# Optimization experiments

Hardware: AMD Instinct MI355X
Metric: run time of the kernel (lower is better)

## Reference

```python
import jax, jax.numpy as jnp
from jax import lax
import numpy as np

PN_FEAT = 64


def _conv(x, w, b):
    # x: [B,H,W,Cin], w: [kh,kw,Cin,Cout] (SAME padding, stride 1)
    return lax.conv_general_dilated(x, w, (1, 1), 'SAME',
                                    dimension_numbers=('NHWC', 'HWIO', 'NHWC')) + b


def setup_inputs() -> dict:
    key = jax.random.key(0)
    ks = jax.random.split(key, 12)
    B, P, N, C = 4, 5000, 100, 8
    nx = ny = 240
    pillars = jax.random.normal(ks[0], (B, P, N, C), dtype=jnp.float32)
    pillar_idxs = jax.random.randint(ks[1], (B, P, 2), 0, nx).astype(jnp.int32)
    def lin(k, fi, fo):
        return jax.random.normal(k, (fi, fo), dtype=jnp.float32) / np.sqrt(fi).astype(np.float32)
    def cnv(k, kh, kw, ci, co):
        return jax.random.normal(k, (kh, kw, ci, co), dtype=jnp.float32) / np.sqrt(kh * kw * ci).astype(np.float32)
    return {
        'pillars': pillars,
        'pillar_idxs': pillar_idxs,
        'nx': nx,
        'ny': ny,
        # pointnet MLP: 8 -> 64 (tanh) -> 64
        'pn_w0': lin(ks[2], 8, 64), 'pn_b0': jnp.zeros((64,), jnp.float32),
        'pn_w1': lin(ks[3], 64, PN_FEAT), 'pn_b1': jnp.zeros((PN_FEAT,), jnp.float32),
        # resnet costmap CNN: 64 -> 128 (tanh) -> 128 (tanh) -> 1, relu output
        'cw0': cnv(ks[4], 3, 3, PN_FEAT, 128), 'cb0': jnp.zeros((128,), jnp.float32),
        'cw1': cnv(ks[5], 3, 3, 128, 128), 'cb1': jnp.zeros((128,), jnp.float32),
        'cw2': cnv(ks[6], 1, 1, 128, 1), 'cb2': jnp.zeros((1,), jnp.float32),
    }


def reference(pillars, pillar_idxs, nx, ny,
              pn_w0, pn_b0, pn_w1, pn_b1,
              cw0, cb0, cw1, cb1, cw2, cb2):
    VALID_THRESH = 1000000.0
    ACT_SCALE = 1.0
    # mask padded points (norm >= 1e6 means invalid)
    valid = (jnp.linalg.norm(pillars, axis=-1, keepdims=True) < VALID_THRESH).astype(pillars.dtype)
    # per-point MLP: [B,P,N,8] -> [B,P,N,F]
    h = jnp.tanh(pillars @ pn_w0 + pn_b0)
    feat = h @ pn_w1 + pn_b1
    # masked max over points in each pillar -> [B,P,F]
    pmax = jnp.max(feat * valid, axis=-2)
    # scatter pillar features into BEV pseudo-image [B,nx,ny,F]
    B = pillars.shape[0]
    bidx = jnp.arange(B)[:, None]                      # [B,1]
    img = jnp.zeros((B, nx, ny, PN_FEAT), pillars.dtype)
    img = img.at[bidx, pillar_idxs[..., 0], pillar_idxs[..., 1]].set(pmax)
    # costmap CNN head (NHWC internally; original is NCHW, same math)
    x = jnp.tanh(_conv(img, cw0, cb0))
    x = jnp.tanh(_conv(x, cw1, cb1))
    x = _conv(x, cw2, cb2)
    return jax.nn.relu(x) * ACT_SCALE            # [B,nx,ny,1]
```

## Files before the change

kernel.cpp:

```cpp
#include <hip/hip_runtime.h>
#include <hip/hip_bf16.h>
#include <math.h>

#define B  4
#define P  5000
#define NPT 100
#define F  64
#define NX 240
#define NY 240
#define C1 128

typedef __attribute__((ext_vector_type(8)))  short short8;
typedef __attribute__((ext_vector_type(16))) float f32x16;

__device__ __forceinline__ float tanh_fast(float x) {
    float e = __expf(2.0f * x);
    float r = __builtin_amdgcn_rcpf(e + 1.0f);
    return __builtin_fmaf(-2.0f, r, 1.0f);
}
__device__ __forceinline__ short bf16_bits(float f) {
    return (short)(__bfloat16_as_ushort(__float2bfloat16(f)));
}

__global__ __launch_bounds__(128) void pn_mfma_kernel(
    const float* __restrict__ pillars,
    const float* __restrict__ w0,
    const float* __restrict__ b0,
    const __hip_bfloat16* __restrict__ w1t,
    const float* __restrict__ b1,
    float* __restrict__ pmax)
{
    constexpr int HS = F + 8;
    constexpr int XS = 32;
    __shared__ short xA[128 * XS];
    __shared__ short hA[128 * HS];
    __shared__ float vmask[128];
    __shared__ float red[2][F];

    int bp = blockIdx.x;
    int n  = threadIdx.x;
    bool live = (n < NPT);

    const float* xp = pillars + ((size_t)bp * NPT + (live ? n : 0)) * 8;
    float4 q0 = *(const float4*)xp;
    float4 q1 = *(const float4*)(xp + 4);
    float x[8] = {q0.x, q0.y, q0.z, q0.w, q1.x, q1.y, q1.z, q1.w};

    float ss = 0.f;
#pragma unroll
    for (int c = 0; c < 8; c++) ss += x[c] * x[c];
    vmask[n] = live ? ((ss < 1e12f) ? 1.0f : 0.0f) : -1.0f;

    short8 xhi, xlo, xz;
#pragma unroll
    for (int c = 0; c < 8; c++) {
        __hip_bfloat16 hb = __float2bfloat16(x[c]);
        float hv = __bfloat162float(hb);
        xhi[c] = (short)__bfloat16_as_ushort(hb);
        xlo[c] = bf16_bits(x[c] - hv);
        xz[c] = 0;
    }
    *(short8*)&xA[n * XS + 0]  = xhi;
    *(short8*)&xA[n * XS + 8]  = xlo;
    *(short8*)&xA[n * XS + 16] = xhi;
    *(short8*)&xA[n * XS + 24] = xz;
    __syncthreads();

    int wave = n >> 6, lane = n & 63;
    int mr = lane & 31;
    int g  = lane >> 5;

    short8 wb[2][2];
#pragma unroll
    for (int nt = 0; nt < 2; nt++) {
        int nn = nt * 32 + mr;
#pragma unroll
        for (int j = 0; j < 8; j++) {
            float wv = w0[j * F + nn];
            __hip_bfloat16 hb = __float2bfloat16(wv);
            wb[0][nt][j] = (short)__bfloat16_as_ushort(hb);
            wb[1][nt][j] = (g == 0) ? bf16_bits(wv - __bfloat162float(hb)) : (short)0;
        }
    }

    f32x16 hc00 = {0,0,0,0,0,0,0,0,0,0,0,0,0,0,0,0};
    f32x16 hc01 = hc00, hc10 = hc00, hc11 = hc00;
#pragma unroll
    for (int kk = 0; kk < 2; kk++) {
        short8 a0 = *(const short8*)&xA[(wave * 64 + mr) * XS + kk * 16 + g * 8];
        short8 a1 = *(const short8*)&xA[(wave * 64 + 32 + mr) * XS + kk * 16 + g * 8];
        hc00 = __builtin_amdgcn_mfma_f32_32x32x16_bf16(a0, wb[kk][0], hc00, 0, 0, 0);
        hc01 = __builtin_amdgcn_mfma_f32_32x32x16_bf16(a0, wb[kk][1], hc01, 0, 0, 0);
        hc10 = __builtin_amdgcn_mfma_f32_32x32x16_bf16(a1, wb[kk][0], hc10, 0, 0, 0);
        hc11 = __builtin_amdgcn_mfma_f32_32x32x16_bf16(a1, wb[kk][1], hc11, 0, 0, 0);
    }

    float b00 = b0[mr];
    float b01 = b0[32 + mr];
#pragma unroll
    for (int mt = 0; mt < 2; mt++) {
#pragma unroll
        for (int r = 0; r < 16; r++) {
            int prow = wave * 64 + mt * 32 + (r & 3) + 8 * (r >> 2) + 4 * g;
            float h0 = (mt == 0) ? hc00[r] : hc10[r];
            float h1 = (mt == 0) ? hc01[r] : hc11[r];
            hA[prow * HS + mr]      = bf16_bits(tanh_fast(h0 + b00));
            hA[prow * HS + 32 + mr] = bf16_bits(tanh_fast(h1 + b01));
        }
    }
    __syncthreads();

    short8 bfrag[2][4];
#pragma unroll
    for (int nt = 0; nt < 2; nt++)
#pragma unroll
        for (int c0 = 0; c0 < 4; c0++)
            bfrag[nt][c0] = *(const short8*)((const short*)w1t +
                                (nt * 32 + mr) * F + c0 * 16 + g * 8);

    f32x16 acc00 = {0,0,0,0,0,0,0,0,0,0,0,0,0,0,0,0};
    f32x16 acc01 = acc00, acc10 = acc00, acc11 = acc00;

    const short* arow = &hA[(wave * 64 + mr) * HS + g * 8];
#pragma unroll
    for (int c0 = 0; c0 < 4; c0++) {
        short8 af0 = *(const short8*)(arow + c0 * 16);
        short8 af1 = *(const short8*)(arow + 32 * HS + c0 * 16);
        acc00 = __builtin_amdgcn_mfma_f32_32x32x16_bf16(af0, bfrag[0][c0], acc00, 0, 0, 0);
        acc01 = __builtin_amdgcn_mfma_f32_32x32x16_bf16(af0, bfrag[1][c0], acc01, 0, 0, 0);
        acc10 = __builtin_amdgcn_mfma_f32_32x32x16_bf16(af1, bfrag[0][c0], acc10, 0, 0, 0);
        acc11 = __builtin_amdgcn_mfma_f32_32x32x16_bf16(af1, bfrag[1][c0], acc11, 0, 0, 0);
    }

    float bv0 = b1[mr];
    float bv1 = b1[32 + mr];
    float mx0 = -INFINITY, mx1 = -INFINITY;
#pragma unroll
    for (int mt = 0; mt < 2; mt++) {
#pragma unroll
        for (int r = 0; r < 16; r++) {
            int row = (r & 3) + 8 * (r >> 2) + 4 * g;
            int p = wave * 64 + mt * 32 + row;
            float vm = vmask[p];
            float a0 = (mt == 0) ? acc00[r] : acc10[r];
            float a1 = (mt == 0) ? acc01[r] : acc11[r];
            float v0 = (vm < 0.f) ? -INFINITY : (a0 + bv0) * vm;
            float v1 = (vm < 0.f) ? -INFINITY : (a1 + bv1) * vm;
            mx0 = fmaxf(mx0, v0);
            mx1 = fmaxf(mx1, v1);
        }
    }
    mx0 = fmaxf(mx0, __shfl_xor(mx0, 32, 64));
    mx1 = fmaxf(mx1, __shfl_xor(mx1, 32, 64));
    if (lane < 32) { red[wave][mr] = mx0; red[wave][32 + mr] = mx1; }
    __syncthreads();
    if (n < F)
        pmax[(size_t)bp * F + n] = fmaxf(red[0][n], red[1][n]);
}

__global__ __launch_bounds__(256) void winner_kernel(
    const int* __restrict__ idxs, int* __restrict__ winner)
{
    int i = blockIdx.x * 256 + threadIdx.x;
    if (i >= B * P) return;
    int ix = idxs[i * 2], iy = idxs[i * 2 + 1];
    int b = i / P, p = i % P;
    atomicMax(&winner[(b * NX + ix) * NY + iy], p);
}

__global__ __launch_bounds__(64) void scatter_kernel(
    const int* __restrict__ idxs, const int* __restrict__ winner,
    const float* __restrict__ pmax, __hip_bfloat16* __restrict__ img)
{
    int bp = blockIdx.x;
    int f = threadIdx.x;
    int ix = idxs[bp * 2], iy = idxs[bp * 2 + 1];
    int b = bp / P, p = bp % P;
    int cell = (b * NX + ix) * NY + iy;
    if (winner[cell] == p)
        img[(size_t)cell * F + f] = __float2bfloat16(pmax[(size_t)bp * F + f]);
}

__global__ __launch_bounds__(256) void cvt_w_kernel(
    const float* __restrict__ w, __hip_bfloat16* __restrict__ wt, int cin)
{
    int idx = blockIdx.x * 256 + threadIdx.x;
    int total = 9 * cin * 128;
    if (idx >= total) return;
    int co = idx % 128;
    int rest = idx / 128;
    int ci = rest % cin;
    int t  = rest / cin;
    int c0 = ci >> 4, c16 = ci & 15;
    wt[(((size_t)(t * (cin >> 4) + c0)) * 128 + co) * 16 + c16] = __float2bfloat16(w[idx]);
}

__global__ __launch_bounds__(256) void cvt_w1_kernel(
    const float* __restrict__ w1, __hip_bfloat16* __restrict__ w1t)
{
    int idx = blockIdx.x * 256 + threadIdx.x;
    if (idx >= F * F) return;
    int k = idx >> 6, nn = idx & 63;
    w1t[nn * F + k] = __float2bfloat16(w1[idx]);
}

template<int CIN, bool FUSE>
__global__ __launch_bounds__(256) void conv_mfma(
    const __hip_bfloat16* __restrict__ in,
    const __hip_bfloat16* __restrict__ wt,
    const float* __restrict__ bias,
    const float* __restrict__ w2,
    const float* __restrict__ b2,
    __hip_bfloat16* __restrict__ out_bf,
    float* __restrict__ out_f)
{
    constexpr int CPAD = CIN + 8;
    constexpr int NC16 = CIN / 16;
    constexpr int NC8  = CIN / 8;
    __shared__ __hip_bfloat16 sP[4 * 66 * CPAD];
    __shared__ float sred[4][64];

    int tid  = threadIdx.x;
    int wave = tid >> 6;
    int lane = tid & 63;
    int mr = lane & 31;
    int g  = lane >> 5;
    int xr  = wave & 1;
    int coh = wave >> 1;
    int y0 = blockIdx.x * 64;
    int x0 = blockIdx.y * 2;
    int b  = blockIdx.z;
    int n0 = coh * 64;

    for (int t = tid; t < 4 * 66 * NC8; t += 256) {
        int c8  = t & (NC8 - 1);
        int row = t / NC8;
        int dy  = row % 66;
        int dx  = row / 66;
        int gx = x0 + dx - 1, gy = y0 + dy - 1;
        float4 v = make_float4(0.f, 0.f, 0.f, 0.f);
        if (gx >= 0 && gx < NX && gy >= 0 && gy < NY)
            v = *(const float4*)&in[(((size_t)b * NX + gx) * NY + gy) * CIN + c8 * 8];
        *(float4*)&sP[row * CPAD + c8 * 8] = v;
    }

    const short* wts = (const short*)wt;
    short8 wbuf[2][NC16][2];
#pragma unroll
    for (int c0 = 0; c0 < NC16; c0++)
#pragma unroll
        for (int nt = 0; nt < 2; nt++)
            wbuf[0][c0][nt] = *(const short8*)(wts +
                ((size_t)c0 * 128 + n0 + nt * 32 + mr) * 16 + g * 8);

    __syncthreads();

    f32x16 acc00 = {0,0,0,0,0,0,0,0,0,0,0,0,0,0,0,0};
    f32x16 acc01 = acc00, acc10 = acc00, acc11 = acc00;
    const short* sPs = (const short*)sP;

#pragma unroll
    for (int tap = 0; tap < 9; tap++) {
        int kh = tap / 3, kw = tap % 3;
        int cur = tap & 1;
        if (tap < 8) {
#pragma unroll
            for (int c0 = 0; c0 < NC16; c0++)
#pragma unroll
                for (int nt = 0; nt < 2; nt++)
                    wbuf[cur ^ 1][c0][nt] = *(const short8*)(wts +
                        ((size_t)((tap + 1) * NC16 + c0) * 128 + n0 + nt * 32 + mr) * 16 + g * 8);
        }
        int prow = ((xr + kh) * 66 + kw + mr) * CPAD + g * 8;
#pragma unroll
        for (int c0 = 0; c0 < NC16; c0++) {
            short8 a0 = *(const short8*)(sPs + prow + c0 * 16);
            short8 a1 = *(const short8*)(sPs + prow + 32 * CPAD + c0 * 16);
            acc00 = __builtin_amdgcn_mfma_f32_32x32x16_bf16(a0, wbuf[cur][c0][0], acc00, 0, 0, 0);
            acc01 = __builtin_amdgcn_mfma_f32_32x32x16_bf16(a0, wbuf[cur][c0][1], acc01, 0, 0, 0);
            acc10 = __builtin_amdgcn_mfma_f32_32x32x16_bf16(a1, wbuf[cur][c0][0], acc10, 0, 0, 0);
            acc11 = __builtin_amdgcn_mfma_f32_32x32x16_bf16(a1, wbuf[cur][c0][1], acc11, 0, 0, 0);
        }
    }

    float bv0 = bias[n0 + mr];
    float bv1 = bias[n0 + 32 + mr];
    int gx = x0 + xr;
    if (!FUSE) {
        size_t base = (((size_t)b * NX + gx) * NY);
#pragma unroll
        for (int mt = 0; mt < 2; mt++) {
#pragma unroll
            for (int r = 0; r < 16; r++) {
                float a0 = (mt == 0) ? acc00[r] : acc10[r];
                float a1 = (mt == 0) ? acc01[r] : acc11[r];
                int row = (r & 3) + 8 * (r >> 2) + 4 * g;
                int y = y0 + mt * 32 + row;
                if (y < NY) {
                    out_bf[(base + y) * C1 + n0 + mr]      = __float2bfloat16(tanh_fast(a0 + bv0));
                    out_bf[(base + y) * C1 + n0 + 32 + mr] = __float2bfloat16(tanh_fast(a1 + bv1));
                }
            }
        }
    } else {
        float w20 = w2[n0 + mr];
        float w21 = w2[n0 + 32 + mr];
#pragma unroll
        for (int mt = 0; mt < 2; mt++) {
#pragma unroll
            for (int r = 0; r < 16; r++) {
                float a0 = (mt == 0) ? acc00[r] : acc10[r];
                float a1 = (mt == 0) ? acc01[r] : acc11[r];
                float v = tanh_fast(a0 + bv0) * w20 + tanh_fast(a1 + bv1) * w21;
                v += __shfl_xor(v, 1, 64);
                v += __shfl_xor(v, 2, 64);
                v += __shfl_xor(v, 4, 64);
                v += __shfl_xor(v, 8, 64);
                v += __shfl_xor(v, 16, 64);
                if (mr == 0) {
                    int row = (r & 3) + 8 * (r >> 2) + 4 * g;
                    sred[wave][mt * 32 + row] = v;
                }
            }
        }
        __syncthreads();
        if (tid < 128) {
            int xr2 = tid >> 6;
            int yy  = tid & 63;
            int y = y0 + yy;
            if (y < NY) {
                float r = sred[xr2][yy] + sred[2 + xr2][yy] + b2[0];
                out_f[((size_t)b * NX + x0 + xr2) * NY + y] = fmaxf(r, 0.f);
            }
        }
    }
}

extern "C" void kernel_launch(void* const* d_in, const int* in_sizes, int n_in,
                              void* d_out, int out_size, void* d_ws, size_t ws_size,
                              hipStream_t stream) {
    const float* pillars = (const float*)d_in[0];
    const int*   idxs    = (const int*)d_in[1];
    const float* pn_w0   = (const float*)d_in[4];
    const float* pn_b0   = (const float*)d_in[5];
    const float* pn_w1   = (const float*)d_in[6];
    const float* pn_b1   = (const float*)d_in[7];
    const float* cw0     = (const float*)d_in[8];
    const float* cb0     = (const float*)d_in[9];
    const float* cw1     = (const float*)d_in[10];
    const float* cb1     = (const float*)d_in[11];
    const float* cw2     = (const float*)d_in[12];
    const float* cb2     = (const float*)d_in[13];
    float* out = (float*)d_out;

    char* ws = (char*)d_ws;
    const size_t IMG_BYTES  = (size_t)B * NX * NY * F * 2;
    const size_t OUT1_BYTES = (size_t)B * NX * NY * C1 * 2;
    const size_t WIN_BYTES  = (size_t)B * NX * NY * 4;
    const size_t PMAX_BYTES = (size_t)B * P * F * 4;
    const size_t WT1_BYTES  = (size_t)9 * C1 * F * 2;
    const size_t WT2_BYTES  = (size_t)9 * C1 * C1 * 2;
    __hip_bfloat16* img  = (__hip_bfloat16*)ws;
    __hip_bfloat16* out1 = (__hip_bfloat16*)(ws + IMG_BYTES);
    int*   winner = (int*)(ws + IMG_BYTES + OUT1_BYTES);
    float* pmax   = (float*)(ws + IMG_BYTES + OUT1_BYTES + WIN_BYTES);
    __hip_bfloat16* wt1 = (__hip_bfloat16*)(ws + IMG_BYTES + OUT1_BYTES + WIN_BYTES + PMAX_BYTES);
    __hip_bfloat16* wt2 = (__hip_bfloat16*)(ws + IMG_BYTES + OUT1_BYTES + WIN_BYTES + PMAX_BYTES + WT1_BYTES);
    __hip_bfloat16* w1t = (__hip_bfloat16*)(ws + IMG_BYTES + OUT1_BYTES + WIN_BYTES + PMAX_BYTES + WT1_BYTES + WT2_BYTES);

    hipMemsetAsync(img, 0, IMG_BYTES, stream);
    hipMemsetAsync(winner, 0xFF, WIN_BYTES, stream);

    cvt_w_kernel<<<(9 * F * C1 + 255) / 256, 256, 0, stream>>>(cw0, wt1, F);
    cvt_w_kernel<<<(9 * C1 * C1 + 255) / 256, 256, 0, stream>>>(cw1, wt2, C1);
    cvt_w1_kernel<<<(F * F + 255) / 256, 256, 0, stream>>>(pn_w1, w1t);

    pn_mfma_kernel<<<B * P, 128, 0, stream>>>(pillars, pn_w0, pn_b0, w1t, pn_b1, pmax);
    winner_kernel<<<(B * P + 255) / 256, 256, 0, stream>>>(idxs, winner);
    scatter_kernel<<<B * P, 64, 0, stream>>>(idxs, winner, pmax, img);

    conv_mfma<F, false><<<dim3(4, NX / 2, B), 256, 0, stream>>>(
        img, wt1, cb0, nullptr, nullptr, out1, nullptr);
    conv_mfma<C1, true><<<dim3(4, NX / 2, B), 256, 0, stream>>>(
        out1, wt2, cb1, cw2, cb2, nullptr, out);
}
```

Baseline: 391.7 us.

## Retile conv kernels to 128-row wave tiles with channel-split LDS passes

Each wave now accumulates a 128x64 output tile (4x2 MFMA accumulators) instead of 64x64, so every weight fragment loaded from global memory feeds twice as many MFMAs. The input halo is staged in LDS in 64-channel passes, which keeps LDS at about 75 KB per block even for the 128-channel conv, and launch_bounds asks for 2 blocks per CU. The grid becomes 120x2 blocks, each covering 112-row-strided y windows of 128 rows, so rows 112-127 are computed twice and the bounds checks are dropped. The trade-off is higher register pressure from 8 accumulators and an extra barrier and reload between channel passes.

```diff
diff --git a/kernel.cpp b/kernel.cpp
--- a/kernel.cpp
+++ b/kernel.cpp
@@ -205,7 +205,7 @@
 }
 
 template<int CIN, bool FUSE>
-__global__ __launch_bounds__(256) void conv_mfma(
+__global__ __launch_bounds__(256, 2) void conv_mfma(
     const __hip_bfloat16* __restrict__ in,
     const __hip_bfloat16* __restrict__ wt,
     const float* __restrict__ bias,
@@ -214,124 +214,131 @@
     __hip_bfloat16* __restrict__ out_bf,
     float* __restrict__ out_f)
 {
-    constexpr int CPAD = CIN + 8;
-    constexpr int NC16 = CIN / 16;
-    constexpr int NC8  = CIN / 8;
-    __shared__ __hip_bfloat16 sP[4 * 66 * CPAD];
-    __shared__ float sred[4][64];
+    constexpr int PASSES = CIN / 64;
+    constexpr int CI   = 64;
+    constexpr int CPAD = CI + 8;
+    constexpr int NC16 = CI / 16;
+    constexpr int NC8  = CI / 8;
+    constexpr int ROWS = 4 * 130;
+    __shared__ short sP[ROWS * CPAD];
+    __shared__ float sred[FUSE ? 2 : 1][2][128];
 
     int tid  = threadIdx.x;
     int wave = tid >> 6;
     int lane = tid & 63;
     int mr = lane & 31;
     int g  = lane >> 5;
-    int xr  = wave & 1;
-    int coh = wave >> 1;
-    int y0 = blockIdx.x * 64;
-    int x0 = blockIdx.y * 2;
+    int coh = wave & 1;
+    int xr  = wave >> 1;
+    int x0 = blockIdx.x * 2;
+    int y0 = blockIdx.y * 112;
     int b  = blockIdx.z;
     int n0 = coh * 64;
 
-    for (int t = tid; t < 4 * 66 * NC8; t += 256) {
-        int c8  = t & (NC8 - 1);
-        int row = t / NC8;
-        int dy  = row % 66;
-        int dx  = row / 66;
-        int gx = x0 + dx - 1, gy = y0 + dy - 1;
-        float4 v = make_float4(0.f, 0.f, 0.f, 0.f);
-        if (gx >= 0 && gx < NX && gy >= 0 && gy < NY)
-            v = *(const float4*)&in[(((size_t)b * NX + gx) * NY + gy) * CIN + c8 * 8];
-        *(float4*)&sP[row * CPAD + c8 * 8] = v;
-    }
-
     const short* wts = (const short*)wt;
+
+    f32x16 acc[4][2];
+#pragma unroll
+    for (int mt = 0; mt < 4; mt++)
+#pragma unroll
+        for (int nt = 0; nt < 2; nt++)
+            acc[mt][nt] = (f32x16){0,0,0,0,0,0,0,0,0,0,0,0,0,0,0,0};
+
     short8 wbuf[2][NC16][2];
 #pragma unroll
     for (int c0 = 0; c0 < NC16; c0++)
 #pragma unroll
         for (int nt = 0; nt < 2; nt++)
             wbuf[0][c0][nt] = *(const short8*)(wts +
-                ((size_t)c0 * 128 + n0 + nt * 32 + mr) * 16 + g * 8);
-
-    __syncthreads();
-
-    f32x16 acc00 = {0,0,0,0,0,0,0,0,0,0,0,0,0,0,0,0};
-    f32x16 acc01 = acc00, acc10 = acc00, acc11 = acc00;
-    const short* sPs = (const short*)sP;
-
-#pragma unroll
-    for (int tap = 0; tap < 9; tap++) {
-        int kh = tap / 3, kw = tap % 3;
-        int cur = tap & 1;
-        if (tap < 8) {
-#pragma unroll
-            for (int c0 = 0; c0 < NC16; c0++)
-#pragma unroll
-                for (int nt = 0; nt < 2; nt++)
-                    wbuf[cur ^ 1][c0][nt] = *(const short8*)(wts +
-                        ((size_t)((tap + 1) * NC16 + c0) * 128 + n0 + nt * 32 + mr) * 16 + g * 8);
-        }
-        int prow = ((xr + kh) * 66 + kw + mr) * CPAD + g * 8;
-#pragma unroll
-        for (int c0 = 0; c0 < NC16; c0++) {
-            short8 a0 = *(const short8*)(sPs + prow + c0 * 16);
-            short8 a1 = *(const short8*)(sPs + prow + 32 * CPAD + c0 * 16);
-            acc00 = __builtin_amdgcn_mfma_f32_32x32x16_bf16(a0, wbuf[cur][c0][0], acc00, 0, 0, 0);
-            acc01 = __builtin_amdgcn_mfma_f32_32x32x16_bf16(a0, wbuf[cur][c0][1], acc01, 0, 0, 0);
-            acc10 = __builtin_amdgcn_mfma_f32_32x32x16_bf16(a1, wbuf[cur][c0][0], acc10, 0, 0, 0);
-            acc11 = __builtin_amdgcn_mfma_f32_32x32x16_bf16(a1, wbuf[cur][c0][1], acc11, 0, 0, 0);
+                ((0 * (CIN / 16) + c0) * 128 + n0 + nt * 32 + mr) * 16 + g * 8);
+
+#pragma unroll
+    for (int p = 0; p < PASSES; p++) {
+        if (p) __syncthreads();
+
+#pragma unroll 4
+        for (int i = 0; i < 17; i++) {
+            int t = tid + i * 256;
+            if (t < ROWS * NC8) {
+                int c8 = t & (NC8 - 1);
+                int r  = t >> 3;
+                int dx = r / 130, dy = r - dx * 130;
+                int gx = x0 - 1 + dx, gy = y0 - 1 + dy;
+                float4 v = make_float4(0.f, 0.f, 0.f, 0.f);
+                if (gx >= 0 && gx < NX && gy >= 0 && gy < NY)
+                    v = *(const float4*)&in[(((size_t)b * NX + gx) * NY + gy) * CIN + p * CI + c8 * 8];
+                *(float4*)&sP[r * CPAD + c8 * 8] = v;
+            }
+        }
+        __syncthreads();
+
+#pragma unroll
+        for (int tap = 0; tap < 9; tap++) {
+            int s = p * 9 + tap;
+            int cur = s & 1;
+            if (s + 1 < 9 * PASSES) {
+                int sn = s + 1, pn_ = sn / 9, tn = sn % 9;
+#pragma unroll
+                for (int c0 = 0; c0 < NC16; c0++)
+#pragma unroll
+                    for (int nt = 0; nt < 2; nt++)
+                        wbuf[cur ^ 1][c0][nt] = *(const short8*)(wts +
+                            ((tn * (CIN / 16) + pn_ * NC16 + c0) * 128 + n0 + nt * 32 + mr) * 16 + g * 8);
+            }
+            int kh = tap / 3, kw = tap % 3;
+            const short* abase = sP + ((xr + kh) * 130 + kw + mr) * CPAD + g * 8;
+#pragma unroll
+            for (int c0 = 0; c0 < NC16; c0++) {
+                short8 a[4];
+#pragma unroll
+                for (int mt = 0; mt < 4; mt++)
+                    a[mt] = *(const short8*)(abase + mt * 32 * CPAD + c0 * 16);
+#pragma unroll
+                for (int mt = 0; mt < 4; mt++) {
+                    acc[mt][0] = __builtin_amdgcn_mfma_f32_32x32x16_bf16(a[mt], wbuf[cur][c0][0], acc[mt][0], 0, 0, 0);
+                    acc[mt][1] = __builtin_amdgcn_mfma_f32_32x32x16_bf16(a[mt], wbuf[cur][c0][1], acc[mt][1], 0, 0, 0);
+                }
+            }
         }
     }
 
     float bv0 = bias[n0 + mr];
     float bv1 = bias[n0 + 32 + mr];
-    int gx = x0 + xr;
     if (!FUSE) {
-        size_t base = (((size_t)b * NX + gx) * NY);
-#pragma unroll
-        for (int mt = 0; mt < 2; mt++) {
+        size_t base = ((size_t)b * NX + (x0 + xr)) * NY;
+#pragma unroll
+        for (int mt = 0; mt < 4; mt++) {
 #pragma unroll
             for (int r = 0; r < 16; r++) {
-                float a0 = (mt == 0) ? acc00[r] : acc10[r];
-                float a1 = (mt == 0) ? acc01[r] : acc11[r];
-                int row = (r & 3) + 8 * (r >> 2) + 4 * g;
-                int y = y0 + mt * 32 + row;
-                if (y < NY) {
-                    out_bf[(base + y) * C1 + n0 + mr]      = __float2bfloat16(tanh_fast(a0 + bv0));
-                    out_bf[(base + y) * C1 + n0 + 32 + mr] = __float2bfloat16(tanh_fast(a1 + bv1));
-                }
+                int y = y0 + mt * 32 + (r & 3) + 8 * (r >> 2) + 4 * g;
+                out_bf[(base + y) * C1 + n0 + mr]      = __float2bfloat16(tanh_fast(acc[mt][0][r] + bv0));
+                out_bf[(base + y) * C1 + n0 + 32 + mr] = __float2bfloat16(tanh_fast(acc[mt][1][r] + bv1));
             }
         }
     } else {
         float w20 = w2[n0 + mr];
         float w21 = w2[n0 + 32 + mr];
 #pragma unroll
-        for (int mt = 0; mt < 2; mt++) {
+        for (int mt = 0; mt < 4; mt++) {
 #pragma unroll
             for (int r = 0; r < 16; r++) {
-                float a0 = (mt == 0) ? acc00[r] : acc10[r];
-                float a1 = (mt == 0) ? acc01[r] : acc11[r];
-                float v = tanh_fast(a0 + bv0) * w20 + tanh_fast(a1 + bv1) * w21;
+                float v = tanh_fast(acc[mt][0][r] + bv0) * w20
+                        + tanh_fast(acc[mt][1][r] + bv1) * w21;
                 v += __shfl_xor(v, 1, 64);
                 v += __shfl_xor(v, 2, 64);
                 v += __shfl_xor(v, 4, 64);
                 v += __shfl_xor(v, 8, 64);
                 v += __shfl_xor(v, 16, 64);
-                if (mr == 0) {
-                    int row = (r & 3) + 8 * (r >> 2) + 4 * g;
-                    sred[wave][mt * 32 + row] = v;
-                }
+                if (mr == 0)
+                    sred[coh][xr][mt * 32 + (r & 3) + 8 * (r >> 2) + 4 * g] = v;
             }
         }
         __syncthreads();
-        if (tid < 128) {
-            int xr2 = tid >> 6;
-            int yy  = tid & 63;
-            int y = y0 + yy;
-            if (y < NY) {
-                float r = sred[xr2][yy] + sred[2 + xr2][yy] + b2[0];
-                out_f[((size_t)b * NX + x0 + xr2) * NY + y] = fmaxf(r, 0.f);
-            }
+        {
+            int row = tid & 127;
+            int xr2 = tid >> 7;
+            float r = sred[0][xr2][row] + sred[1][xr2][row] + b2[0];
+            out_f[((size_t)b * NX + (x0 + xr2)) * NY + (y0 + row)] = fmaxf(r, 0.f);
         }
     }
 }
@@ -379,8 +386,8 @@
     winner_kernel<<<(B * P + 255) / 256, 256, 0, stream>>>(idxs, winner);
     scatter_kernel<<<B * P, 64, 0, stream>>>(idxs, winner, pmax, img);
 
-    conv_mfma<F, false><<<dim3(4, NX / 2, B), 256, 0, stream>>>(
+    conv_mfma<F, false><<<dim3(NX / 2, 2, B), 256, 0, stream>>>(
         img, wt1, cb0, nullptr, nullptr, out1, nullptr);
-    conv_mfma<C1, true><<<dim3(4, NX / 2, B), 256, 0, stream>>>(
+    conv_mfma<C1, true><<<dim3(NX / 2, 2, B), 256, 0, stream>>>(
         out1, wt2, cb1, cw2, cb2, nullptr, out);
 }
```

New measurement: 375.6 us. -4.1%, faster.
